# Performance work log

Hardware: AMD Instinct MI355X
Metric: run time of the kernel (lower is better)

## Reference

```python
import jax, jax.numpy as jnp
import numpy as np

B, S, D, H = 2, 2048, 1024, 16
Dh = D // H
LN_EPS = 1e-5


def setup_inputs() -> dict:
    key = jax.random.key(0)
    ks = jax.random.split(key, 14)
    s = 1.0 / np.sqrt(D)
    return {
        "q": jax.random.normal(ks[0], (B, S, D), jnp.float32),
        "k": jax.random.normal(ks[1], (B, S, D), jnp.float32),
        "v": jax.random.normal(ks[2], (B, S, D), jnp.float32),
        "attn_mask": jax.random.randint(ks[3], (B, S, S), 0, 2).astype(bool),
        "Wq": jax.random.normal(ks[4], (D, D), jnp.float32) * s,
        "bq": jnp.zeros((D,), jnp.float32),
        "Wk": jax.random.normal(ks[5], (D, D), jnp.float32) * s,
        "bk": jnp.zeros((D,), jnp.float32),
        "Wv": jax.random.normal(ks[6], (D, D), jnp.float32) * s,
        "bv": jnp.zeros((D,), jnp.float32),
        "Wo": jax.random.normal(ks[7], (D, D), jnp.float32) * s,
        "bo": jnp.zeros((D,), jnp.float32),
        "gamma": jnp.ones((D,), jnp.float32),
        "beta": jnp.zeros((D,), jnp.float32),
    }


def reference(q, k, v, attn_mask, Wq, bq, Wk, bk, Wv, bv, Wo, bo, gamma, beta):
    residual = q
    # projections (W stored as [in, out])
    qh = (q @ Wq + bq).reshape(B, S, H, Dh).transpose(0, 2, 1, 3)  # [B,H,S,Dh]
    kh = (k @ Wk + bk).reshape(B, S, H, Dh).transpose(0, 2, 1, 3)
    vh = (v @ Wv + bv).reshape(B, S, H, Dh).transpose(0, 2, 1, 3)
    scores = jnp.einsum("bhqd,bhkd->bhqk", qh, kh) / np.sqrt(Dh)
    scores = jnp.where(attn_mask[:, None, :, :], -1e9, scores)
    attn = jax.nn.softmax(scores, axis=-1)  # dropout is identity in eval
    context = jnp.einsum("bhqk,bhkd->bhqd", attn, vh)  # [B,H,S,Dh]
    # faithful to original bug: flat reshape WITHOUT transposing heads back
    context = context.reshape(B, S, D)
    out = context @ Wo + bo
    x = residual + out
    mu = jnp.mean(x, axis=-1, keepdims=True)
    var = jnp.var(x, axis=-1, keepdims=True)
    out = (x - mu) / jnp.sqrt(var + LN_EPS) * gamma + beta
    return out, attn
```

## Files before the change

### kernel.cpp

```cpp
#include <hip/hip_runtime.h>
#include <hip/hip_bf16.h>

typedef __attribute__((ext_vector_type(8))) short bf16x8;
typedef __attribute__((ext_vector_type(4))) float f32x4;

__device__ __forceinline__ short f2bf(float f) {
    union { float f; unsigned u; } v; v.f = f;
    unsigned r = (v.u + 0x7FFFu + ((v.u >> 16) & 1u)) >> 16;
    return (short)r;
}
__device__ __forceinline__ float bf2f(short s) {
    union { unsigned u; float f; } v; v.u = ((unsigned)(unsigned short)s) << 16;
    return v.f;
}
__device__ __forceinline__ void gll16(const void* g, void* l) {
    __builtin_amdgcn_global_load_lds(
        (const __attribute__((address_space(1))) unsigned int*)g,
        (__attribute__((address_space(3))) unsigned int*)l, 16, 0, 0);
}

#define QSCALE 0.18033688011112042f

__global__ __launch_bounds__(256) void k_prep(
    const float* __restrict__ qin, const float* __restrict__ kin, const float* __restrict__ vin,
    short* __restrict__ qbf, short* __restrict__ kbf, short* __restrict__ vbf,
    const float* __restrict__ Wq, const float* __restrict__ Wk,
    const float* __restrict__ Wv, const float* __restrict__ Wo,
    short* __restrict__ WqT, short* __restrict__ WkT,
    short* __restrict__ WvT, short* __restrict__ WoT,
    const int* __restrict__ mask, unsigned* __restrict__ mb)
{
    __shared__ int sm[8192];
    const int bid = blockIdx.x, tid = threadIdx.x;
    if (bid < 6144) {
        const float* in = bid < 2048 ? qin : (bid < 4096 ? kin : vin);
        short* out = bid < 2048 ? qbf : (bid < 4096 ? kbf : vbf);
        const long i = ((long)(bid & 2047) * 256 + tid) * 8;
        float4 f0 = *reinterpret_cast<const float4*>(&in[i]);
        float4 f1 = *reinterpret_cast<const float4*>(&in[i + 4]);
        bf16x8 v;
        v[0] = f2bf(f0.x); v[1] = f2bf(f0.y); v[2] = f2bf(f0.z); v[3] = f2bf(f0.w);
        v[4] = f2bf(f1.x); v[5] = f2bf(f1.y); v[6] = f2bf(f1.z); v[7] = f2bf(f1.w);
        *reinterpret_cast<bf16x8*>(&out[i]) = v;
    } else if (bid < 10240) {
        const int t2 = bid - 6144, which = t2 >> 10, local = t2 & 1023;
        const float* W = which == 0 ? Wq : (which == 1 ? Wk : (which == 2 ? Wv : Wo));
        short* WT = which == 0 ? WqT : (which == 1 ? WkT : (which == 2 ? WvT : WoT));
        float (*t)[33] = reinterpret_cast<float(*)[33]>(sm);
        const int rb = (local >> 5) * 32, cb = (local & 31) * 32;
        const int tr = tid >> 3, tc = (tid & 7) * 4;
        const float4 v = *reinterpret_cast<const float4*>(&W[(long)(rb + tr) * 1024 + cb + tc]);
        t[tr][tc + 0] = v.x; t[tr][tc + 1] = v.y; t[tr][tc + 2] = v.z; t[tr][tc + 3] = v.w;
        __syncthreads();
        short4 o;
        o.x = f2bf(t[tc + 0][tr]); o.y = f2bf(t[tc + 1][tr]);
        o.z = f2bf(t[tc + 2][tr]); o.w = f2bf(t[tc + 3][tr]);
        *reinterpret_cast<short4*>(&WT[(long)(cb + tr) * 1024 + rb + tc]) = o;
    } else {
        const long base = (long)(bid - 10240) * 8192;
#pragma unroll
        for (int i = 0; i < 8; ++i)
            *reinterpret_cast<int4*>(&sm[i * 1024 + tid * 4]) =
                *reinterpret_cast<const int4*>(&mask[base + i * 1024 + tid * 4]);
        __syncthreads();
        unsigned wv = 0;
#pragma unroll
        for (int j = 0; j < 32; ++j) wv |= (sm[tid * 32 + j] != 0 ? 1u : 0u) << j;
        mb[base / 32 + tid] = wv;
    }
}

__global__ __launch_bounds__(256) void k_gemm_qkv(
    const short* __restrict__ A0, const short* __restrict__ A1, const short* __restrict__ A2,
    const short* __restrict__ B0, const short* __restrict__ B1, const short* __restrict__ B2,
    const float* __restrict__ b0, const float* __restrict__ b1, const float* __restrict__ b2,
    short* __restrict__ o0, short* __restrict__ o1, short* __restrict__ o2)
{
    __shared__ short As[128 * 64];
    __shared__ short Bs[128 * 64];
    const int z = blockIdx.z;
    const short* A = z == 0 ? A0 : (z == 1 ? A1 : A2);
    const short* BT = z == 0 ? B0 : (z == 1 ? B1 : B2);
    const float* bias = z == 0 ? b0 : (z == 1 ? b1 : b2);
    short* outp = z == 0 ? o0 : (z == 1 ? o1 : o2);
    const float scale = z == 0 ? QSCALE : 1.0f;

    const int tid = threadIdx.x, w = tid >> 6, lane = tid & 63;
    const int lr = lane & 15, lg = lane >> 4;
    const int rowbase = blockIdx.y * 128, colbase = blockIdx.x * 128;
    const int wr = (w >> 1) * 64, wc = (w & 1) * 64;
    const int srow = lane >> 3, sc_ = (lane & 7) ^ srow;

    f32x4 acc[4][4] = {};

    for (int kb = 0; kb < 1024; kb += 64) {
#pragma unroll
        for (int ii = 0; ii < 4; ++ii) {
            const int rl = w * 32 + ii * 8 + srow;
            gll16(A + (long)(rowbase + rl) * 1024 + kb + sc_ * 8, &As[(w * 32 + ii * 8) * 64]);
            gll16(BT + (long)(colbase + rl) * 1024 + kb + sc_ * 8, &Bs[(w * 32 + ii * 8) * 64]);
        }
        __syncthreads();
#pragma unroll
        for (int ks = 0; ks < 2; ++ks) {
            bf16x8 a[4], bq[4];
#pragma unroll
            for (int m = 0; m < 4; ++m) {
                const int r = wr + m * 16 + lr;
                a[m] = *reinterpret_cast<const bf16x8*>(&As[r * 64 + (((ks * 4 + lg) ^ (r & 7)) << 3)]);
            }
#pragma unroll
            for (int n = 0; n < 4; ++n) {
                const int r = wc + n * 16 + lr;
                bq[n] = *reinterpret_cast<const bf16x8*>(&Bs[r * 64 + (((ks * 4 + lg) ^ (r & 7)) << 3)]);
            }
#pragma unroll
            for (int m = 0; m < 4; ++m)
#pragma unroll
                for (int n = 0; n < 4; ++n)
                    acc[m][n] = __builtin_amdgcn_mfma_f32_16x16x32_bf16(a[m], bq[n], acc[m][n], 0, 0, 0);
        }
        __syncthreads();
    }

#pragma unroll
    for (int m = 0; m < 4; ++m) {
#pragma unroll
        for (int n = 0; n < 4; ++n) {
            const int C = colbase + wc + n * 16 + lr;
            const float bv = bias[C];
            if (z != 2) {
#pragma unroll
                for (int rr = 0; rr < 4; ++rr) {
                    const int R = rowbase + wr + m * 16 + lg * 4 + rr;
                    const float val = (acc[m][n][rr] + bv) * scale;
                    const int b = R >> 11, s = R & 2047, h = C >> 6, dh = C & 63;
                    outp[(((long)(b * 16 + h) * 2048 + s) << 6) + dh] = f2bf(val);
                }
            } else {
                const int R0 = rowbase + wr + m * 16 + lg * 4;
                const int b = R0 >> 11, s0 = R0 & 2047, h = C >> 6, dh = C & 63;
                short4 o;
                o.x = f2bf(acc[m][n][0] + bv);
                o.y = f2bf(acc[m][n][1] + bv);
                o.z = f2bf(acc[m][n][2] + bv);
                o.w = f2bf(acc[m][n][3] + bv);
                *reinterpret_cast<short4*>(&outp[(((long)(b * 16 + h) * 64 + dh) << 11) + s0]) = o;
            }
        }
    }
}

__global__ __launch_bounds__(256) void k_gemm_o(
    const short* __restrict__ A, const short* __restrict__ BT,
    const float* __restrict__ bias, const float* __restrict__ resid,
    float* __restrict__ outp)
{
    __shared__ short As[128 * 64];
    __shared__ short Bs[128 * 64];
    const int tid = threadIdx.x, w = tid >> 6, lane = tid & 63;
    const int lr = lane & 15, lg = lane >> 4;
    const int rowbase = blockIdx.y * 128, colbase = blockIdx.x * 128;
    const int wr = (w >> 1) * 64, wc = (w & 1) * 64;
    const int srow = lane >> 3, sc_ = (lane & 7) ^ srow;

    f32x4 acc[4][4] = {};

    for (int kb = 0; kb < 1024; kb += 64) {
#pragma unroll
        for (int ii = 0; ii < 4; ++ii) {
            const int rl = w * 32 + ii * 8 + srow;
            gll16(A + (long)(rowbase + rl) * 1024 + kb + sc_ * 8, &As[(w * 32 + ii * 8) * 64]);
            gll16(BT + (long)(colbase + rl) * 1024 + kb + sc_ * 8, &Bs[(w * 32 + ii * 8) * 64]);
        }
        __syncthreads();
#pragma unroll
        for (int ks = 0; ks < 2; ++ks) {
            bf16x8 a[4], bq[4];
#pragma unroll
            for (int m = 0; m < 4; ++m) {
                const int r = wr + m * 16 + lr;
                a[m] = *reinterpret_cast<const bf16x8*>(&As[r * 64 + (((ks * 4 + lg) ^ (r & 7)) << 3)]);
            }
#pragma unroll
            for (int n = 0; n < 4; ++n) {
                const int r = wc + n * 16 + lr;
                bq[n] = *reinterpret_cast<const bf16x8*>(&Bs[r * 64 + (((ks * 4 + lg) ^ (r & 7)) << 3)]);
            }
#pragma unroll
            for (int m = 0; m < 4; ++m)
#pragma unroll
                for (int n = 0; n < 4; ++n)
                    acc[m][n] = __builtin_amdgcn_mfma_f32_16x16x32_bf16(a[m], bq[n], acc[m][n], 0, 0, 0);
        }
        __syncthreads();
    }

#pragma unroll
    for (int m = 0; m < 4; ++m) {
#pragma unroll
        for (int n = 0; n < 4; ++n) {
            const int C = colbase + wc + n * 16 + lr;
            const float bv = bias[C];
#pragma unroll
            for (int rr = 0; rr < 4; ++rr) {
                const int R = rowbase + wr + m * 16 + lg * 4 + rr;
                const long idx = (long)R * 1024 + C;
                outp[idx] = acc[m][n][rr] + bv + resid[idx];
            }
        }
    }
}

__global__ __launch_bounds__(256, 4) void k_attn(
    const short* __restrict__ qh, const short* __restrict__ kh,
    const short* __restrict__ vt, const unsigned* __restrict__ mbits,
    float* __restrict__ attn_out, short* __restrict__ ctxb)
{
    const int g = blockIdx.x, xcd = g & 7, u = g >> 3;
    const int bh = u >> 2, qt = xcd * 4 + (u & 3);
    const int b = bh >> 4;
    const int tid = threadIdx.x, w = tid >> 6, lane = tid & 63;
    const int lr = lane & 15, lg = lane >> 4;
    const int irow = qt * 64 + w * 16;
    const long arow = (long)bh * 2048 + irow;

    __shared__ short KV[4][64 * 64];
    __shared__ short Ps[4][16 * 64];

    const short* qhp = qh + arow * 64;
    const short* khp = kh + (long)bh * 131072;
    const short* vtp = vt + (long)bh * 131072;
    const unsigned* mbp = mbits + (long)b * 131072 + (long)irow * 64;

    const bf16x8 aq0 = *reinterpret_cast<const bf16x8*>(&qhp[lr * 64 + lg * 8]);
    const bf16x8 aq1 = *reinterpret_cast<const bf16x8*>(&qhp[lr * 64 + 32 + lg * 8]);
    const int srow = lane >> 3, sc_ = (lane & 7) ^ srow;

    auto stage_k = [&](int buf, int ch) {
#pragma unroll
        for (int ii = 0; ii < 2; ++ii) {
            const int r0 = w * 16 + ii * 8;
            gll16(khp + (long)(ch * 64 + r0 + srow) * 64 + sc_ * 8, &KV[buf][r0 * 64]);
        }
    };
    auto stage_v = [&](int buf, int ch) {
#pragma unroll
        for (int ii = 0; ii < 2; ++ii) {
            const int r0 = w * 16 + ii * 8;
            gll16(vtp + (long)(r0 + srow) * 2048 + ch * 64 + sc_ * 8, &KV[2 + buf][r0 * 64]);
        }
    };
    auto kfrag = [&](int buf, int t, int ks) -> bf16x8 {
        const int r = t * 16 + lr;
        return *reinterpret_cast<const bf16x8*>(&KV[buf][r * 64 + (((ks * 4 + lg) ^ (r & 7)) << 3)]);
    };
    auto vfrag = [&](int buf, int gi, int ks) -> bf16x8 {
        const int r = gi * 16 + lr;
        return *reinterpret_cast<const bf16x8*>(&KV[2 + buf][r * 64 + (((ks * 4 + lg) ^ (r & 7)) << 3)]);
    };
    auto ps_write = [&](int row, int t, float p) {
        const int ch8 = (t * 2 + (lr >> 3)) ^ (row & 7);
        Ps[w][row * 64 + (ch8 << 3) + (lr & 7)] = f2bf(p);
    };

    float l[4] = {0.f, 0.f, 0.f, 0.f};
    f32x4 acc[4] = {};

    stage_k(0, 0); stage_v(0, 0);
    asm volatile("s_waitcnt vmcnt(0)" ::: "memory");
    __builtin_amdgcn_s_barrier();
    asm volatile("" ::: "memory");

    for (int ch = 0; ch < 32; ++ch) {
        const int cur = ch & 1;
        unsigned mw[4][2];
#pragma unroll
        for (int rr = 0; rr < 4; ++rr) {
            mw[rr][0] = mbp[(lg * 4 + rr) * 64 + ch * 2];
            mw[rr][1] = mbp[(lg * 4 + rr) * 64 + ch * 2 + 1];
        }
        asm volatile("" ::: "memory");
        if (ch < 31) { stage_k(cur ^ 1, ch + 1); stage_v(cur ^ 1, ch + 1); }
        asm volatile("" ::: "memory");

#pragma unroll
        for (int t = 0; t < 4; ++t) {
            f32x4 sc = {};
            sc = __builtin_amdgcn_mfma_f32_16x16x32_bf16(aq0, kfrag(cur, t, 0), sc, 0, 0, 0);
            sc = __builtin_amdgcn_mfma_f32_16x16x32_bf16(aq1, kfrag(cur, t, 1), sc, 0, 0, 0);
#pragma unroll
            for (int rr = 0; rr < 4; ++rr) {
                const bool masked = (mw[rr][t >> 1] >> (((t & 1) << 4) + lr)) & 1;
                const float p = exp2f(masked ? -1e9f : sc[rr]);
                l[rr] += p;
                ps_write(lg * 4 + rr, t, p);
            }
        }
        const bf16x8 pa0 = *reinterpret_cast<const bf16x8*>(&Ps[w][lr * 64 + (((0 * 4 + lg) ^ (lr & 7)) << 3)]);
        const bf16x8 pa1 = *reinterpret_cast<const bf16x8*>(&Ps[w][lr * 64 + (((1 * 4 + lg) ^ (lr & 7)) << 3)]);
#pragma unroll
        for (int gi = 0; gi < 4; ++gi) {
            acc[gi] = __builtin_amdgcn_mfma_f32_16x16x32_bf16(pa0, vfrag(cur, gi, 0), acc[gi], 0, 0, 0);
            acc[gi] = __builtin_amdgcn_mfma_f32_16x16x32_bf16(pa1, vfrag(cur, gi, 1), acc[gi], 0, 0, 0);
        }
        asm volatile("s_waitcnt vmcnt(0)" ::: "memory");
        __builtin_amdgcn_s_barrier();
        asm volatile("" ::: "memory");
    }

    float C[4];
#pragma unroll
    for (int rr = 0; rr < 4; ++rr) {
#pragma unroll
        for (int off = 1; off < 16; off <<= 1) l[rr] += __shfl_xor(l[rr], off, 16);
        l[rr] = fmaxf(l[rr], 1e-30f);
        C[rr] = log2f(l[rr]);
    }
#pragma unroll
    for (int gi = 0; gi < 4; ++gi)
#pragma unroll
        for (int rr = 0; rr < 4; ++rr)
            ctxb[(arow + lg * 4 + rr) * 64 + gi * 16 + lr] = f2bf(acc[gi][rr] / l[rr]);

    auto emit_chunk = [&](int ch, unsigned (&mw)[4][2]) {
        const int buf = ch & 3;
#pragma unroll
        for (int t = 0; t < 4; ++t) {
            f32x4 sc = {};
            sc = __builtin_amdgcn_mfma_f32_16x16x32_bf16(aq0, kfrag(buf, t, 0), sc, 0, 0, 0);
            sc = __builtin_amdgcn_mfma_f32_16x16x32_bf16(aq1, kfrag(buf, t, 1), sc, 0, 0, 0);
#pragma unroll
            for (int rr = 0; rr < 4; ++rr) {
                const bool masked = (mw[rr][t >> 1] >> (((t & 1) << 4) + lr)) & 1;
                const float p = exp2f((masked ? -1e9f : sc[rr]) - C[rr]);
                ps_write(lg * 4 + rr, t, p);
            }
        }
#pragma unroll
        for (int i2 = 0; i2 < 4; ++i2) {
            const int r = i2 * 4 + lg;
            const short4 p4 = *reinterpret_cast<const short4*>(
                &Ps[w][r * 64 + ((((lr >> 1)) ^ (r & 7)) << 3) + ((lr & 1) << 2)]);
            float4 o;
            o.x = bf2f(p4.x); o.y = bf2f(p4.y); o.z = bf2f(p4.z); o.w = bf2f(p4.w);
            *reinterpret_cast<float4*>(&attn_out[(arow + r) * 2048 + ch * 64 + lr * 4]) = o;
        }
    };

    stage_k(0, 0); stage_k(1, 1);
    asm volatile("s_waitcnt vmcnt(0)" ::: "memory");
    __builtin_amdgcn_s_barrier();
    asm volatile("" ::: "memory");

    for (int it = 0; it < 16; ++it) {
        const int chA = it * 2, chB = chA + 1;
        unsigned mwA[4][2], mwB[4][2];
#pragma unroll
        for (int rr = 0; rr < 4; ++rr) {
            mwA[rr][0] = mbp[(lg * 4 + rr) * 64 + chA * 2];
            mwA[rr][1] = mbp[(lg * 4 + rr) * 64 + chA * 2 + 1];
            mwB[rr][0] = mbp[(lg * 4 + rr) * 64 + chB * 2];
            mwB[rr][1] = mbp[(lg * 4 + rr) * 64 + chB * 2 + 1];
        }
        asm volatile("" ::: "memory");
        stage_k((chA + 2) & 3, (chA + 2) & 31);
        stage_k((chB + 2) & 3, (chB + 2) & 31);
        asm volatile("" ::: "memory");

        emit_chunk(chA, mwA);
        emit_chunk(chB, mwB);

        asm volatile("s_waitcnt vmcnt(8)" ::: "memory");
        __builtin_amdgcn_s_barrier();
        asm volatile("" ::: "memory");
    }
}

__global__ __launch_bounds__(256) void k_ln(const float* __restrict__ x,
    const float* __restrict__ gamma, const float* __restrict__ beta,
    float* __restrict__ out)
{
    __shared__ float red[8];
    const int r = blockIdx.x, tid = threadIdx.x;
    const float4 v = reinterpret_cast<const float4*>(x + (long)r * 1024)[tid];
    float s = v.x + v.y + v.z + v.w;
    float q2 = v.x * v.x + v.y * v.y + v.z * v.z + v.w * v.w;
#pragma unroll
    for (int off = 32; off; off >>= 1) {
        s += __shfl_xor(s, off, 64);
        q2 += __shfl_xor(q2, off, 64);
    }
    if ((tid & 63) == 0) { red[(tid >> 6) * 2] = s; red[(tid >> 6) * 2 + 1] = q2; }
    __syncthreads();
    s = red[0] + red[2] + red[4] + red[6];
    q2 = red[1] + red[3] + red[5] + red[7];
    const float mu = s * (1.0f / 1024.0f);
    const float var = q2 * (1.0f / 1024.0f) - mu * mu;
    const float rs = rsqrtf(var + 1e-5f);
    const float4 gm = reinterpret_cast<const float4*>(gamma)[tid];
    const float4 bb = reinterpret_cast<const float4*>(beta)[tid];
    float4 o;
    o.x = (v.x - mu) * rs * gm.x + bb.x;
    o.y = (v.y - mu) * rs * gm.y + bb.y;
    o.z = (v.z - mu) * rs * gm.z + bb.z;
    o.w = (v.w - mu) * rs * gm.w + bb.w;
    reinterpret_cast<float4*>(out + (long)r * 1024)[tid] = o;
}

extern "C" void kernel_launch(void* const* d_in, const int* in_sizes, int n_in,
                              void* d_out, int out_size, void* d_ws, size_t ws_size,
                              hipStream_t stream)
{
    const float* qin  = (const float*)d_in[0];
    const float* kin  = (const float*)d_in[1];
    const float* vin  = (const float*)d_in[2];
    const int*   mask = (const int*)d_in[3];
    const float* Wq = (const float*)d_in[4];
    const float* bq = (const float*)d_in[5];
    const float* Wk = (const float*)d_in[6];
    const float* bk = (const float*)d_in[7];
    const float* Wv = (const float*)d_in[8];
    const float* bv = (const float*)d_in[9];
    const float* Wo = (const float*)d_in[10];
    const float* bo = (const float*)d_in[11];
    const float* gamma = (const float*)d_in[12];
    const float* beta  = (const float*)d_in[13];

    char* ws = (char*)d_ws;
    short* WqT = (short*)(ws + (0ul  << 20));
    short* WkT = (short*)(ws + (2ul  << 20));
    short* WvT = (short*)(ws + (4ul  << 20));
    short* WoT = (short*)(ws + (6ul  << 20));
    short* qbf = (short*)(ws + (8ul  << 20));
    short* kbf = (short*)(ws + (16ul << 20));
    short* vbf = (short*)(ws + (24ul << 20));
    short* qh  = (short*)(ws + (32ul << 20));
    short* khb = (short*)(ws + (40ul << 20));
    short* vtb = (short*)(ws + (48ul << 20));
    unsigned* mb = (unsigned*)(ws + (56ul << 20));
    short* ctxb = (short*)(ws + (57ul << 20));
    float* xb   = (float*)(ws + (8ul  << 20));

    float* outLN = (float*)d_out;
    float* attnO = (float*)d_out + 4194304;

    const dim3 blk(256);
    k_prep<<<dim3(11264), blk, 0, stream>>>(qin, kin, vin, qbf, kbf, vbf,
                                            Wq, Wk, Wv, Wo, WqT, WkT, WvT, WoT, mask, mb);
    k_gemm_qkv<<<dim3(8, 32, 3), blk, 0, stream>>>(qbf, kbf, vbf, WqT, WkT, WvT,
                                                   bq, bk, bv, qh, khb, vtb);
    k_attn<<<dim3(1024), blk, 0, stream>>>(qh, khb, vtb, mb, attnO, ctxb);
    k_gemm_o<<<dim3(8, 32), blk, 0, stream>>>(ctxb, WoT, bo, qin, xb);
    k_ln<<<dim3(4096), blk, 0, stream>>>(xb, gamma, beta, outLN);
}
```

Measured before the change: 312.8 us.

## Load V fragments directly from global, deepen K pipeline, halve O-GEMM row tile

The attention kernel stops staging V through LDS. Each wave now reads V fragments straight from global memory into registers, and the freed LDS holds a 4-deep K ring buffer. The loop processes two chunks per barrier, which halves the number of barriers. Separately, the output GEMM tile shrinks from 128 to 64 rows, doubling the grid to 512 blocks for better CU occupancy, at the cost of reloading B more often. The risk is that direct global V loads add exposed latency, and the 16 KB V tile is re-read by all four waves.

```diff
diff --git a/kernel.cpp b/kernel.cpp
--- a/kernel.cpp
+++ b/kernel.cpp
@@ -156,29 +156,33 @@
     const float* __restrict__ bias, const float* __restrict__ resid,
     float* __restrict__ outp)
 {
-    __shared__ short As[128 * 64];
+    __shared__ short As[64 * 64];
     __shared__ short Bs[128 * 64];
     const int tid = threadIdx.x, w = tid >> 6, lane = tid & 63;
     const int lr = lane & 15, lg = lane >> 4;
-    const int rowbase = blockIdx.y * 128, colbase = blockIdx.x * 128;
-    const int wr = (w >> 1) * 64, wc = (w & 1) * 64;
+    const int rowbase = blockIdx.y * 64, colbase = blockIdx.x * 128;
+    const int wr = (w >> 1) * 32, wc = (w & 1) * 64;
     const int srow = lane >> 3, sc_ = (lane & 7) ^ srow;
 
-    f32x4 acc[4][4] = {};
+    f32x4 acc[2][4] = {};
 
     for (int kb = 0; kb < 1024; kb += 64) {
+#pragma unroll
+        for (int ii = 0; ii < 2; ++ii) {
+            const int rl = w * 16 + ii * 8 + srow;
+            gll16(A + (long)(rowbase + rl) * 1024 + kb + sc_ * 8, &As[(w * 16 + ii * 8) * 64]);
+        }
 #pragma unroll
         for (int ii = 0; ii < 4; ++ii) {
             const int rl = w * 32 + ii * 8 + srow;
-            gll16(A + (long)(rowbase + rl) * 1024 + kb + sc_ * 8, &As[(w * 32 + ii * 8) * 64]);
             gll16(BT + (long)(colbase + rl) * 1024 + kb + sc_ * 8, &Bs[(w * 32 + ii * 8) * 64]);
         }
         __syncthreads();
 #pragma unroll
         for (int ks = 0; ks < 2; ++ks) {
-            bf16x8 a[4], bq[4];
-#pragma unroll
-            for (int m = 0; m < 4; ++m) {
+            bf16x8 a[2], bq[4];
+#pragma unroll
+            for (int m = 0; m < 2; ++m) {
                 const int r = wr + m * 16 + lr;
                 a[m] = *reinterpret_cast<const bf16x8*>(&As[r * 64 + (((ks * 4 + lg) ^ (r & 7)) << 3)]);
             }
@@ -188,7 +192,7 @@
                 bq[n] = *reinterpret_cast<const bf16x8*>(&Bs[r * 64 + (((ks * 4 + lg) ^ (r & 7)) << 3)]);
             }
 #pragma unroll
-            for (int m = 0; m < 4; ++m)
+            for (int m = 0; m < 2; ++m)
 #pragma unroll
                 for (int n = 0; n < 4; ++n)
                     acc[m][n] = __builtin_amdgcn_mfma_f32_16x16x32_bf16(a[m], bq[n], acc[m][n], 0, 0, 0);
@@ -197,7 +201,7 @@
     }
 
 #pragma unroll
-    for (int m = 0; m < 4; ++m) {
+    for (int m = 0; m < 2; ++m) {
 #pragma unroll
         for (int n = 0; n < 4; ++n) {
             const int C = colbase + wc + n * 16 + lr;
@@ -225,7 +229,7 @@
     const int irow = qt * 64 + w * 16;
     const long arow = (long)bh * 2048 + irow;
 
-    __shared__ short KV[4][64 * 64];
+    __shared__ short Ks[4][64 * 64];
     __shared__ short Ps[4][16 * 64];
 
     const short* qhp = qh + arow * 64;
@@ -241,23 +245,12 @@
 #pragma unroll
         for (int ii = 0; ii < 2; ++ii) {
             const int r0 = w * 16 + ii * 8;
-            gll16(khp + (long)(ch * 64 + r0 + srow) * 64 + sc_ * 8, &KV[buf][r0 * 64]);
-        }
-    };
-    auto stage_v = [&](int buf, int ch) {
-#pragma unroll
-        for (int ii = 0; ii < 2; ++ii) {
-            const int r0 = w * 16 + ii * 8;
-            gll16(vtp + (long)(r0 + srow) * 2048 + ch * 64 + sc_ * 8, &KV[2 + buf][r0 * 64]);
+            gll16(khp + (long)(ch * 64 + r0 + srow) * 64 + sc_ * 8, &Ks[buf][r0 * 64]);
         }
     };
     auto kfrag = [&](int buf, int t, int ks) -> bf16x8 {
         const int r = t * 16 + lr;
-        return *reinterpret_cast<const bf16x8*>(&KV[buf][r * 64 + (((ks * 4 + lg) ^ (r & 7)) << 3)]);
-    };
-    auto vfrag = [&](int buf, int gi, int ks) -> bf16x8 {
-        const int r = gi * 16 + lr;
-        return *reinterpret_cast<const bf16x8*>(&KV[2 + buf][r * 64 + (((ks * 4 + lg) ^ (r & 7)) << 3)]);
+        return *reinterpret_cast<const bf16x8*>(&Ks[buf][r * 64 + (((ks * 4 + lg) ^ (r & 7)) << 3)]);
     };
     auto ps_write = [&](int row, int t, float p) {
         const int ch8 = (t * 2 + (lr >> 3)) ^ (row & 7);
@@ -267,28 +260,13 @@
     float l[4] = {0.f, 0.f, 0.f, 0.f};
     f32x4 acc[4] = {};
 
-    stage_k(0, 0); stage_v(0, 0);
-    asm volatile("s_waitcnt vmcnt(0)" ::: "memory");
-    __builtin_amdgcn_s_barrier();
-    asm volatile("" ::: "memory");
-
-    for (int ch = 0; ch < 32; ++ch) {
-        const int cur = ch & 1;
-        unsigned mw[4][2];
-#pragma unroll
-        for (int rr = 0; rr < 4; ++rr) {
-            mw[rr][0] = mbp[(lg * 4 + rr) * 64 + ch * 2];
-            mw[rr][1] = mbp[(lg * 4 + rr) * 64 + ch * 2 + 1];
-        }
-        asm volatile("" ::: "memory");
-        if (ch < 31) { stage_k(cur ^ 1, ch + 1); stage_v(cur ^ 1, ch + 1); }
-        asm volatile("" ::: "memory");
-
+    auto do_chunk1 = [&](int ch, unsigned (&mw)[4][2]) {
+        const int buf = ch & 3;
 #pragma unroll
         for (int t = 0; t < 4; ++t) {
             f32x4 sc = {};
-            sc = __builtin_amdgcn_mfma_f32_16x16x32_bf16(aq0, kfrag(cur, t, 0), sc, 0, 0, 0);
-            sc = __builtin_amdgcn_mfma_f32_16x16x32_bf16(aq1, kfrag(cur, t, 1), sc, 0, 0, 0);
+            sc = __builtin_amdgcn_mfma_f32_16x16x32_bf16(aq0, kfrag(buf, t, 0), sc, 0, 0, 0);
+            sc = __builtin_amdgcn_mfma_f32_16x16x32_bf16(aq1, kfrag(buf, t, 1), sc, 0, 0, 0);
 #pragma unroll
             for (int rr = 0; rr < 4; ++rr) {
                 const bool masked = (mw[rr][t >> 1] >> (((t & 1) << 4) + lr)) & 1;
@@ -299,11 +277,39 @@
         }
         const bf16x8 pa0 = *reinterpret_cast<const bf16x8*>(&Ps[w][lr * 64 + (((0 * 4 + lg) ^ (lr & 7)) << 3)]);
         const bf16x8 pa1 = *reinterpret_cast<const bf16x8*>(&Ps[w][lr * 64 + (((1 * 4 + lg) ^ (lr & 7)) << 3)]);
+        const short* vc = vtp + ch * 64;
 #pragma unroll
         for (int gi = 0; gi < 4; ++gi) {
-            acc[gi] = __builtin_amdgcn_mfma_f32_16x16x32_bf16(pa0, vfrag(cur, gi, 0), acc[gi], 0, 0, 0);
-            acc[gi] = __builtin_amdgcn_mfma_f32_16x16x32_bf16(pa1, vfrag(cur, gi, 1), acc[gi], 0, 0, 0);
-        }
+            const bf16x8 v0 = *reinterpret_cast<const bf16x8*>(&vc[(long)(gi * 16 + lr) * 2048 + lg * 8]);
+            const bf16x8 v1 = *reinterpret_cast<const bf16x8*>(&vc[(long)(gi * 16 + lr) * 2048 + 32 + lg * 8]);
+            acc[gi] = __builtin_amdgcn_mfma_f32_16x16x32_bf16(pa0, v0, acc[gi], 0, 0, 0);
+            acc[gi] = __builtin_amdgcn_mfma_f32_16x16x32_bf16(pa1, v1, acc[gi], 0, 0, 0);
+        }
+    };
+
+    stage_k(0, 0); stage_k(1, 1);
+    asm volatile("s_waitcnt vmcnt(0)" ::: "memory");
+    __builtin_amdgcn_s_barrier();
+    asm volatile("" ::: "memory");
+
+    for (int it = 0; it < 16; ++it) {
+        const int chA = it * 2, chB = chA + 1;
+        unsigned mwA[4][2], mwB[4][2];
+#pragma unroll
+        for (int rr = 0; rr < 4; ++rr) {
+            mwA[rr][0] = mbp[(lg * 4 + rr) * 64 + chA * 2];
+            mwA[rr][1] = mbp[(lg * 4 + rr) * 64 + chA * 2 + 1];
+            mwB[rr][0] = mbp[(lg * 4 + rr) * 64 + chB * 2];
+            mwB[rr][1] = mbp[(lg * 4 + rr) * 64 + chB * 2 + 1];
+        }
+        asm volatile("" ::: "memory");
+        stage_k((chA + 2) & 3, (chA + 2) & 31);
+        stage_k((chB + 2) & 3, (chB + 2) & 31);
+        asm volatile("" ::: "memory");
+
+        do_chunk1(chA, mwA);
+        do_chunk1(chB, mwB);
+
         asm volatile("s_waitcnt vmcnt(0)" ::: "memory");
         __builtin_amdgcn_s_barrier();
         asm volatile("" ::: "memory");
@@ -451,6 +457,6 @@
     k_gemm_qkv<<<dim3(8, 32, 3), blk, 0, stream>>>(qbf, kbf, vbf, WqT, WkT, WvT,
                                                    bq, bk, bv, qh, khb, vtb);
     k_attn<<<dim3(1024), blk, 0, stream>>>(qh, khb, vtb, mb, attnO, ctxb);
-    k_gemm_o<<<dim3(8, 32), blk, 0, stream>>>(ctxb, WoT, bo, qin, xb);
+    k_gemm_o<<<dim3(8, 64), blk, 0, stream>>>(ctxb, WoT, bo, qin, xb);
     k_ln<<<dim3(4096), blk, 0, stream>>>(xb, gamma, beta, outLN);
 }
```

New measurement: 366.2 us. 17.1% more time.
